# Optimization experiments

Measured on AMD Instinct MI355X. Metric: run time of the kernel, lower is better.

The kernel has to match this reference:

```python
import jax, jax.numpy as jnp
import numpy as np

N = 10000; E = 160000; C = 32; NB = 128; H = 64; L = 3; NL = 4; RC = 5.0
DIMS = [1, 3, 5, 7]

def _sph(v):
    # real spherical harmonics l=0..3 of unit vectors v [E,3]
    x, y, z = v[:, 0], v[:, 1], v[:, 2]
    s3 = 3.0 ** 0.5; s5 = 5.0 ** 0.5; s15 = 15.0 ** 0.5; s7 = 7.0 ** 0.5
    sh0 = jnp.ones_like(x)[:, None]
    sh1 = s3 * v
    sh2 = jnp.stack([s15 * x * y, s15 * y * z, (s5 / 2) * (3 * z * z - 1),
                     s15 * x * z, (s15 / 2) * (x * x - y * y)], -1)
    c1 = (35.0 / 8) ** 0.5; c2 = 105.0 ** 0.5; c3 = (21.0 / 8) ** 0.5; c4 = s7 / 2; c5 = (105.0 ** 0.5) / 2
    sh3 = jnp.stack([c1 * y * (3 * x * x - y * y), c2 * x * y * z, c3 * y * (5 * z * z - 1),
                     c4 * (5 * z ** 3 - 3 * z), c3 * x * (5 * z * z - 1),
                     c5 * z * (x * x - y * y), c1 * x * (x * x - 3 * y * y)], -1)
    return [sh0, sh1, sh2, sh3]

def setup_inputs() -> dict:
    key = jax.random.key(0)
    ks = jax.random.split(key, 14)
    inp = {}
    inp['pos'] = jax.random.uniform(ks[0], (N, 3), jnp.float32) * 10.0  # box of side 10
    inp['node_embed'] = jax.random.normal(ks[1], (4, C), jnp.float32)
    inp['rw1'] = jax.random.normal(ks[2], (NB, H), jnp.float32) * 0.1
    inp['rb1'] = jax.random.normal(ks[3], (H,), jnp.float32) * 0.1
    inp['rw2'] = jax.random.normal(ks[4], (H, L * NL * C), jnp.float32) * 0.1
    inp['rb2'] = jax.random.normal(ks[5], (L * NL * C,), jnp.float32) * 0.1
    inp['self_w'] = jax.random.normal(ks[6], (L, NL, C, C), jnp.float32) * (1.0 / C ** 0.5)
    inp['msg_w'] = jax.random.normal(ks[7], (L, NL, C, C), jnp.float32) * (1.0 / C ** 0.5)
    inp['gate_w'] = jax.random.normal(ks[8], (L, C, C), jnp.float32) * (1.0 / C ** 0.5)
    inp['edge_w'] = jax.random.normal(ks[9], (H, NL * C), jnp.float32) * 0.1
    inp['edge_b'] = jax.random.normal(ks[10], (NL * C,), jnp.float32) * 0.1
    inp['species'] = jax.random.randint(ks[11], (N,), 0, 4)
    inp['edge_index'] = jax.random.randint(ks[12], (2, E), 0, N)
    return inp

def reference(pos, node_embed, rw1, rb1, rw2, rb2, self_w, msg_w, gate_w,
              edge_w, edge_b, species, edge_index):
    src, dst = edge_index[0], edge_index[1]
    vec = pos[dst] - pos[src]                       # [E,3]
    r = jnp.sqrt(jnp.sum(vec * vec, -1) + 1e-12)    # [E]
    u = jnp.clip(r / RC, 0.0, 1.0)
    env = 0.5 * (jnp.cos(jnp.pi * u) + 1.0)         # smooth cutoff, 0 beyond rc
    n = jnp.arange(1, NB + 1, dtype=pos.dtype)
    rb = env[:, None] * (2.0 / RC) ** 0.5 * jnp.sin(jnp.pi * n * u[:, None]) / r[:, None]  # Bessel basis [E,NB]
    h = jax.nn.silu(rb @ rw1 + rb1)                 # [E,H]
    w_all = (h @ rw2 + rb2).reshape(E, L, NL, C)    # per-layer per-l radial weights
    ew = (h @ edge_w + edge_b).reshape(E, NL, C)
    sh = _sph(vec / r[:, None])                     # list of [E, 2l+1]
    # node features per l: [N, C, 2l+1]; l=0 initialized from species embedding
    f = [node_embed[species][:, :, None]] + [jnp.zeros((N, C, d), pos.dtype) for d in DIMS[1:]]
    for t in range(L):
        s = f[0][src][:, :, 0]                      # sender scalars [E,C]
        new = []
        for l in range(NL):
            # scalar-gated radial x SH message (equivariant): [E,C,2l+1]
            m = w_all[:, t, l, :, None] * s[:, :, None] * sh[l][:, None, :]
            agg = jax.ops.segment_sum(m, dst, num_segments=N)
            new.append(jnp.einsum('ncm,cd->ndm', f[l], self_w[t, l]) +
                       jnp.einsum('ncm,cd->ndm', agg, msg_w[t, l]))
        gate = jax.nn.sigmoid(new[0][:, :, 0] @ gate_w[t])  # [N,C]
        f = [jax.nn.silu(new[0])] + [new[l] * gate[:, :, None] for l in range(1, NL)]
    node_out = jnp.concatenate([f[l].reshape(N, C * DIMS[l]) for l in range(NL)], -1)   # [N,512]
    g = f[0][src][:, :, 0] + f[0][dst][:, :, 0]     # [E,C]
    edge_out = jnp.concatenate(
        [(ew[:, l, :, None] * g[:, :, None] * sh[l][:, None, :]).reshape(E, C * DIMS[l])
         for l in range(NL)], -1)                   # [E,512]
    return jnp.concatenate([node_out, edge_out], 0)  # [N+E, 512]
```

## Files before the change

kernel.cpp:

```cpp
#include <hip/hip_runtime.h>

#define NN 10000
#define EE 160000
#define CC 32
#define NBAS 128
#define HH 64
#define LL 3

__device__ __forceinline__ float sigmoidf_(float x) { return 1.0f / (1.0f + expf(-x)); }

__device__ __forceinline__ void edge_geom(const float* pos, int src, int dst,
                                          float& inv_r, float& u, float& pref,
                                          float& x, float& y, float& z) {
    float vx = pos[dst * 3 + 0] - pos[src * 3 + 0];
    float vy = pos[dst * 3 + 1] - pos[src * 3 + 1];
    float vz = pos[dst * 3 + 2] - pos[src * 3 + 2];
    float r2 = vx * vx + vy * vy + vz * vz + 1e-12f;
    float r = sqrtf(r2);
    inv_r = 1.0f / r;
    u = fminf(r * 0.2f, 1.0f);
    const float PI = 3.14159265358979f;
    float env = 0.5f * (cosf(PI * u) + 1.0f);
    pref = env * 0.6324555320336759f * inv_r;
    x = vx * inv_r; y = vy * inv_r; z = vz * inv_r;
}

__device__ __forceinline__ void sph_all(float x, float y, float z, float* shv) {
    const float s3 = 1.7320508075688772f, s5 = 2.23606797749979f, s15 = 3.872983346207417f;
    const float c1 = 2.0916500663351885f;
    const float c2 = 10.246950765959598f;
    const float c3 = 1.6201851746019649f;
    const float c4 = 1.3228756555322954f;
    const float c5 = 5.123475382979799f;
    shv[0] = 1.0f;
    shv[1] = s3 * x; shv[2] = s3 * y; shv[3] = s3 * z;
    shv[4] = s15 * x * y;
    shv[5] = s15 * y * z;
    shv[6] = 0.5f * s5 * (3.0f * z * z - 1.0f);
    shv[7] = s15 * x * z;
    shv[8] = 0.5f * s15 * (x * x - y * y);
    shv[9]  = c1 * y * (3.0f * x * x - y * y);
    shv[10] = c2 * x * y * z;
    shv[11] = c3 * y * (5.0f * z * z - 1.0f);
    shv[12] = c4 * (5.0f * z * z * z - 3.0f * z);
    shv[13] = c3 * x * (5.0f * z * z - 1.0f);
    shv[14] = c5 * z * (x * x - y * y);
    shv[15] = c1 * x * (x * x - 3.0f * y * y);
}

__global__ void k_deg(const int* __restrict__ ei, int* __restrict__ deg) {
    int e = blockIdx.x * blockDim.x + threadIdx.x;
    if (e < EE) atomicAdd(&deg[ei[EE + e]], 1);
}

__global__ __launch_bounds__(256) void k_scan(const int* __restrict__ deg, int* __restrict__ rowptr) {
    __shared__ int part[256];
    const int CHUNK = 40;
    int tid = threadIdx.x;
    int s = 0;
#pragma unroll
    for (int k = 0; k < CHUNK; k++) {
        int idx = tid * CHUNK + k;
        if (idx < NN) s += deg[idx];
    }
    part[tid] = s;
    __syncthreads();
    for (int off = 1; off < 256; off <<= 1) {
        int v = (tid >= off) ? part[tid - off] : 0;
        __syncthreads();
        part[tid] += v;
        __syncthreads();
    }
    int run = (tid > 0) ? part[tid - 1] : 0;
#pragma unroll
    for (int k = 0; k < CHUNK; k++) {
        int idx = tid * CHUNK + k;
        if (idx < NN) { rowptr[idx] = run; run += deg[idx]; }
    }
    if (tid == 255) rowptr[NN] = run;
}

__global__ void k_scatter(const int* __restrict__ ei, const int* __restrict__ rowptr,
                          int* __restrict__ cursor, int* __restrict__ csr) {
    int e = blockIdx.x * blockDim.x + threadIdx.x;
    if (e >= EE) return;
    int d = ei[EE + e];
    int slot = atomicAdd(&cursor[d], 1);
    csr[rowptr[d] + slot] = e;
}

__global__ void k_init_f0(const float* __restrict__ ne, const int* __restrict__ species,
                          float* __restrict__ f0) {
    int idx = blockIdx.x * blockDim.x + threadIdx.x;
    if (idx >= NN * CC) return;
    int c = idx & 31;
    int n = idx >> 5;
    f0[idx] = ne[species[n] * CC + c];
}

__global__ __launch_bounds__(256) void k_edge_pre(
    const float* __restrict__ pos, const float* __restrict__ rw1, const float* __restrict__ rb1,
    const int* __restrict__ ei, float* __restrict__ hbuf, float* __restrict__ shbuf) {
    __shared__ float rw1_s[NBAS * HH];
    __shared__ float rb_s[64 * 132];
    int tid = threadIdx.x;
    int ebase = blockIdx.x * 64;
    for (int i = tid; i < NBAS * HH / 4; i += 256)
        *(float4*)&rw1_s[i * 4] = *(const float4*)&rw1[i * 4];
    {
        int r = tid >> 2, q = tid & 3;
        int e = ebase + r;
        int src = ei[e], dst = ei[EE + e];
        float inv_r, u, pref, x, y, z;
        edge_geom(pos, src, dst, inv_r, u, pref, x, y, z);
        float shv[16];
        sph_all(x, y, z, shv);
        float4 sv;
        sv.x = shv[q * 4 + 0]; sv.y = shv[q * 4 + 1];
        sv.z = shv[q * 4 + 2]; sv.w = shv[q * 4 + 3];
        *(float4*)&shbuf[(size_t)e * 16 + q * 4] = sv;
        const float PI = 3.14159265358979f;
        float th = PI * u;
        float tc = 2.0f * cosf(th);
        float* rp = &rb_s[r * 132 + 32 * q];
        int n0 = 32 * q + 1;
#pragma unroll
        for (int g = 0; g < 2; g++) {
            int nb = n0 + 16 * g;
            float sm1 = sinf(th * (float)nb);
            float s0 = sinf(th * (float)(nb + 1));
            rp[16 * g + 0] = pref * sm1;
            rp[16 * g + 1] = pref * s0;
#pragma unroll
            for (int j = 2; j < 16; j++) {
                float s = tc * s0 - sm1;
                sm1 = s0; s0 = s;
                rp[16 * g + j] = pref * s;
            }
        }
    }
    __syncthreads();
    int col0 = (tid & 15) * 4;
    int r0 = (tid >> 4) * 4;
    float acc[4][4];
#pragma unroll
    for (int i = 0; i < 4; i++) { acc[i][0] = 0.f; acc[i][1] = 0.f; acc[i][2] = 0.f; acc[i][3] = 0.f; }
#pragma unroll 2
    for (int k0 = 0; k0 < NBAS; k0 += 4) {
        float4 w0 = *(float4*)&rw1_s[(k0 + 0) * HH + col0];
        float4 w1 = *(float4*)&rw1_s[(k0 + 1) * HH + col0];
        float4 w2 = *(float4*)&rw1_s[(k0 + 2) * HH + col0];
        float4 w3 = *(float4*)&rw1_s[(k0 + 3) * HH + col0];
#pragma unroll
        for (int i = 0; i < 4; i++) {
            float4 rv = *(float4*)&rb_s[(r0 + i) * 132 + k0];
            acc[i][0] += rv.x * w0.x; acc[i][1] += rv.x * w0.y; acc[i][2] += rv.x * w0.z; acc[i][3] += rv.x * w0.w;
            acc[i][0] += rv.y * w1.x; acc[i][1] += rv.y * w1.y; acc[i][2] += rv.y * w1.z; acc[i][3] += rv.y * w1.w;
            acc[i][0] += rv.z * w2.x; acc[i][1] += rv.z * w2.y; acc[i][2] += rv.z * w2.z; acc[i][3] += rv.z * w2.w;
            acc[i][0] += rv.w * w3.x; acc[i][1] += rv.w * w3.y; acc[i][2] += rv.w * w3.z; acc[i][3] += rv.w * w3.w;
        }
    }
    float4 bv = *(const float4*)&rb1[col0];
#pragma unroll
    for (int i = 0; i < 4; i++) {
        float a0 = acc[i][0] + bv.x, a1 = acc[i][1] + bv.y;
        float a2 = acc[i][2] + bv.z, a3 = acc[i][3] + bv.w;
        float4 hres;
        hres.x = a0 * sigmoidf_(a0); hres.y = a1 * sigmoidf_(a1);
        hres.z = a2 * sigmoidf_(a2); hres.w = a3 * sigmoidf_(a3);
        *(float4*)&hbuf[(size_t)(ebase + r0 + i) * HH + col0] = hres;
    }
}

__global__ __launch_bounds__(256) void k_gemm_all(
    const float* __restrict__ hbuf, const float* __restrict__ rw2,
    const float* __restrict__ rb2, const int* __restrict__ csr,
    float* __restrict__ aw, int panel0, int npanel) {
    __shared__ float w_s[HH * 128];
    __shared__ float h_s[64][68];
    int tid = threadIdx.x;
    int pbase = blockIdx.x * 64;
    {
        int r = tid >> 2, q = tid & 3;
        int e = csr[pbase + r];
        const float4* hp = (const float4*)(hbuf + (size_t)e * HH + q * 16);
        float4 v0 = hp[0], v1 = hp[1], v2 = hp[2], v3 = hp[3];
        float4* dp = (float4*)&h_s[r][q * 16];
        dp[0] = v0; dp[1] = v1; dp[2] = v2; dp[3] = v3;
    }
    int ob = (tid & 31) << 2;
    int r0 = (tid >> 5) << 3;
    for (int p = 0; p < npanel; p++) {
        int wcol = (panel0 + p) * 128;
        __syncthreads();
        for (int i = tid; i < HH * 32; i += 256) {
            int j = i >> 5, o4 = (i & 31) << 2;
            *(float4*)&w_s[j * 128 + o4] = *(const float4*)&rw2[(size_t)j * 384 + wcol + o4];
        }
        __syncthreads();
        float acc[8][4];
#pragma unroll
        for (int i = 0; i < 8; i++) { acc[i][0] = 0.f; acc[i][1] = 0.f; acc[i][2] = 0.f; acc[i][3] = 0.f; }
#pragma unroll 2
        for (int k0 = 0; k0 < HH; k0 += 4) {
            float4 w0 = *(float4*)&w_s[(k0 + 0) * 128 + ob];
            float4 w1 = *(float4*)&w_s[(k0 + 1) * 128 + ob];
            float4 w2 = *(float4*)&w_s[(k0 + 2) * 128 + ob];
            float4 w3 = *(float4*)&w_s[(k0 + 3) * 128 + ob];
#pragma unroll
            for (int i = 0; i < 8; i++) {
                float4 hv = *(float4*)&h_s[r0 + i][k0];
                acc[i][0] += hv.x * w0.x; acc[i][1] += hv.x * w0.y; acc[i][2] += hv.x * w0.z; acc[i][3] += hv.x * w0.w;
                acc[i][0] += hv.y * w1.x; acc[i][1] += hv.y * w1.y; acc[i][2] += hv.y * w1.z; acc[i][3] += hv.y * w1.w;
                acc[i][0] += hv.z * w2.x; acc[i][1] += hv.z * w2.y; acc[i][2] += hv.z * w2.z; acc[i][3] += hv.z * w2.w;
                acc[i][0] += hv.w * w3.x; acc[i][1] += hv.w * w3.y; acc[i][2] += hv.w * w3.z; acc[i][3] += hv.w * w3.w;
            }
        }
        float4 bv = *(const float4*)&rb2[wcol + ob];
        float* awp = aw + (size_t)p * EE * 128;
#pragma unroll
        for (int i = 0; i < 8; i++) {
            float4 res;
            res.x = acc[i][0] + bv.x; res.y = acc[i][1] + bv.y;
            res.z = acc[i][2] + bv.z; res.w = acc[i][3] + bv.w;
            *(float4*)&awp[(size_t)(pbase + r0 + i) * 128 + ob] = res;
        }
    }
}

template<int INIT, int FINAL>
__global__ __launch_bounds__(256) void k_aggnode(
    const float* __restrict__ aw, const float* __restrict__ shbuf,
    const float* __restrict__ f0prev, const float* __restrict__ f_cur,
    const int* __restrict__ ei, const int* __restrict__ rowptr,
    const int* __restrict__ csr,
    const float* __restrict__ self_w, const float* __restrict__ msg_w,
    const float* __restrict__ gate_w,
    float* __restrict__ f_next, float* __restrict__ f0_out, int t) {
    __shared__ float agg_s[4][CC * 17];
    __shared__ float new_s[4][CC * 17];
    __shared__ float gate_s[4][CC];
    int w = threadIdx.x >> 6, lane = threadIdx.x & 63;
    int n = blockIdx.x * 4 + w;
    int c = lane & 31;
    int half = lane >> 5;
    float acc0[3] = {0.f, 0.f, 0.f};
    float acc1[7] = {0.f, 0.f, 0.f, 0.f, 0.f, 0.f, 0.f};
    int beg = rowptr[n], end = rowptr[n + 1];
    for (int k = beg; k < end; k++) {
        int e = csr[k];
        int src = ei[e];
        float fs = f0prev[src * CC + c];
        float a0 = aw[(size_t)k * 128 + lane] * fs;
        float a1 = aw[(size_t)k * 128 + 64 + lane] * fs;
        const float4* shp = (const float4*)(shbuf + (size_t)e * 16);
        float4 s0 = shp[0], s1 = shp[1], s2 = shp[2], s3 = shp[3];
        if (half == 0) {
            acc0[0] += a0 * s0.x;
            acc1[0] += a1 * s1.x; acc1[1] += a1 * s1.y;
            acc1[2] += a1 * s1.z; acc1[3] += a1 * s1.w; acc1[4] += a1 * s2.x;
        } else {
            acc0[0] += a0 * s0.y; acc0[1] += a0 * s0.z; acc0[2] += a0 * s0.w;
            acc1[0] += a1 * s2.y; acc1[1] += a1 * s2.z; acc1[2] += a1 * s2.w;
            acc1[3] += a1 * s3.x; acc1[4] += a1 * s3.y; acc1[5] += a1 * s3.z; acc1[6] += a1 * s3.w;
        }
    }
    {
        int l0 = half, dl0 = 2 * l0 + 1, mo0 = l0 * l0;
        int l1 = 2 + half, dl1 = 2 * l1 + 1, mo1 = l1 * l1;
        float* ap = &agg_s[w][c * 17];
#pragma unroll
        for (int m = 0; m < 3; m++)
            if (m < dl0) ap[mo0 + m] = acc0[m];
#pragma unroll
        for (int m = 0; m < 7; m++)
            if (m < dl1) ap[mo1 + m] = acc1[m];
    }
    int d = c, mg = half;
#pragma unroll
    for (int k = 0; k < 8; k++) {
        int m = mg + 2 * k;
        int l = (m == 0) ? 0 : (m < 4) ? 1 : (m < 9) ? 2 : 3;
        const float* sw = self_w + (size_t)((t * 4 + l) * CC) * CC + d;
        const float* mw = msg_w + (size_t)((t * 4 + l) * CC) * CC + d;
        float acc = 0.0f;
#pragma unroll 8
        for (int c2 = 0; c2 < CC; c2++) {
            float fv;
            if (INIT) fv = (m == 0) ? f0prev[n * CC + c2] : 0.0f;
            else fv = f_cur[((size_t)n * CC + c2) * 16 + m];
            acc += fv * sw[c2 * CC] + agg_s[w][c2 * 17 + m] * mw[c2 * CC];
        }
        new_s[w][d * 17 + m] = acc;
    }
    if (mg == 0) {
        float g = 0.0f;
#pragma unroll 8
        for (int c2 = 0; c2 < CC; c2++)
            g += new_s[w][c2 * 17 + 0] * gate_w[((size_t)t * CC + c2) * CC + d];
        gate_s[w][d] = sigmoidf_(g);
    }
#pragma unroll
    for (int k = 0; k < 8; k++) {
        int m = mg + 2 * k;
        float v = new_s[w][d * 17 + m];
        if (m == 0) v = v * sigmoidf_(v);
        else v *= gate_s[w][d];
        if (FINAL) {
            int l = (m == 0) ? 0 : (m < 4) ? 1 : (m < 9) ? 2 : 3;
            f_next[(size_t)n * 512 + 32 * l * l + d * (2 * l + 1) + (m - l * l)] = v;
        } else {
            f_next[((size_t)n * CC + d) * 16 + m] = v;
        }
        if (m == 0) f0_out[n * CC + d] = v;
    }
}

template<int DL>
__device__ __forceinline__ void emit_edge(float* outp, const float* shp,
                                          float e0, float e1, float e2, float e3) {
    float ew[4] = {e0, e1, e2, e3};
    float buf[4 * DL];
#pragma unroll
    for (int cc = 0; cc < 4; cc++)
#pragma unroll
        for (int m = 0; m < DL; m++) buf[cc * DL + m] = ew[cc] * shp[m];
#pragma unroll
    for (int t = 0; t < DL; t++) *(float4*)&outp[t * 4] = *(float4*)&buf[t * 4];
}

__global__ __launch_bounds__(256) void k_edge_out(
    const float* __restrict__ hbuf, const float* __restrict__ shbuf,
    const float* __restrict__ edge_w, const float* __restrict__ edge_b,
    const float* __restrict__ f0, const int* __restrict__ ei,
    float* __restrict__ out) {
    __shared__ float w_s[HH * 128];
    __shared__ float h_s[64][68];
    __shared__ float sh_s[64][16];
    int tid = threadIdx.x;
    int ebase = blockIdx.x * 64;
    for (int i = tid; i < HH * 32; i += 256) {
        int j = i >> 5, o4 = (i & 31) << 2;
        *(float4*)&w_s[j * 128 + o4] = *(const float4*)&edge_w[(size_t)j * 128 + o4];
    }
    {
        int r = tid >> 2, q = tid & 3;
        int e = ebase + r;
        const float4* hp = (const float4*)(hbuf + (size_t)e * HH + q * 16);
        float4 v0 = hp[0], v1 = hp[1], v2 = hp[2], v3 = hp[3];
        float4* dp = (float4*)&h_s[r][q * 16];
        dp[0] = v0; dp[1] = v1; dp[2] = v2; dp[3] = v3;
        *(float4*)&sh_s[r][q * 4] = *(const float4*)&shbuf[(size_t)e * 16 + q * 4];
    }
    __syncthreads();
    int ob = (tid & 31) << 2;
    int r0 = (tid >> 5) << 3;
    float acc[8][4];
#pragma unroll
    for (int i = 0; i < 8; i++) { acc[i][0] = 0.f; acc[i][1] = 0.f; acc[i][2] = 0.f; acc[i][3] = 0.f; }
#pragma unroll 2
    for (int k0 = 0; k0 < HH; k0 += 4) {
        float4 w0 = *(float4*)&w_s[(k0 + 0) * 128 + ob];
        float4 w1 = *(float4*)&w_s[(k0 + 1) * 128 + ob];
        float4 w2 = *(float4*)&w_s[(k0 + 2) * 128 + ob];
        float4 w3 = *(float4*)&w_s[(k0 + 3) * 128 + ob];
#pragma unroll
        for (int i = 0; i < 8; i++) {
            float4 hv = *(float4*)&h_s[r0 + i][k0];
            acc[i][0] += hv.x * w0.x; acc[i][1] += hv.x * w0.y; acc[i][2] += hv.x * w0.z; acc[i][3] += hv.x * w0.w;
            acc[i][0] += hv.y * w1.x; acc[i][1] += hv.y * w1.y; acc[i][2] += hv.y * w1.z; acc[i][3] += hv.y * w1.w;
            acc[i][0] += hv.z * w2.x; acc[i][1] += hv.z * w2.y; acc[i][2] += hv.z * w2.z; acc[i][3] += hv.z * w2.w;
            acc[i][0] += hv.w * w3.x; acc[i][1] += hv.w * w3.y; acc[i][2] += hv.w * w3.z; acc[i][3] += hv.w * w3.w;
        }
    }
    float4 bv = *(const float4*)&edge_b[ob];
    int l = ob >> 5;
    int cbase = ob & 31;
    int dl = 2 * l + 1, mo = l * l, co = 32 * l * l;
#pragma unroll
    for (int i = 0; i < 8; i++) {
        int rr = r0 + i;
        int e = ebase + rr;
        int src = ei[e], dst = ei[EE + e];
        float4 g1 = *(const float4*)&f0[src * CC + cbase];
        float4 g2 = *(const float4*)&f0[dst * CC + cbase];
        float e0 = (acc[i][0] + bv.x) * (g1.x + g2.x);
        float e1 = (acc[i][1] + bv.y) * (g1.y + g2.y);
        float e2 = (acc[i][2] + bv.z) * (g1.z + g2.z);
        float e3 = (acc[i][3] + bv.w) * (g1.w + g2.w);
        float* outp = out + ((size_t)NN + e) * 512 + co + (size_t)cbase * dl;
        const float* shp = &sh_s[rr][mo];
        if (l == 0)      emit_edge<1>(outp, shp, e0, e1, e2, e3);
        else if (l == 1) emit_edge<3>(outp, shp, e0, e1, e2, e3);
        else if (l == 2) emit_edge<5>(outp, shp, e0, e1, e2, e3);
        else             emit_edge<7>(outp, shp, e0, e1, e2, e3);
    }
}

__global__ __launch_bounds__(256) void k_out_edge(
    const float* __restrict__ pos, const float* __restrict__ rw1, const float* __restrict__ rb1,
    const float* __restrict__ edge_w, const float* __restrict__ edge_b,
    const float* __restrict__ f0, const int* __restrict__ ei, float* __restrict__ out) {
    __shared__ float rw1_s[NBAS * HH];
    __shared__ float ew_s[HH * 128];
    __shared__ float rb_s[4][NBAS];
    __shared__ float h_s[4][HH];
    __shared__ float g_s[4][CC];
    __shared__ float sh_s[4][16];
    int tid = threadIdx.x;
    for (int i = tid; i < NBAS * HH; i += 256) rw1_s[i] = rw1[i];
    for (int i = tid; i < HH * 128; i += 256) ew_s[i] = edge_w[i];
    int w = tid >> 6, lane = tid & 63;
    int e = blockIdx.x * 4 + w;
    int src = ei[e], dst = ei[EE + e];
    float inv_r, u, pref, x, y, z;
    edge_geom(pos, src, dst, inv_r, u, pref, x, y, z);
    const float PI = 3.14159265358979f;
#pragma unroll
    for (int rep = 0; rep < 2; rep++) {
        int k = lane + rep * 64;
        rb_s[w][k] = pref * sinf(PI * (float)(k + 1) * u);
    }
    float shv[16];
    sph_all(x, y, z, shv);
    if (lane < 16) {
        float v = shv[0];
#pragma unroll
        for (int k = 1; k < 16; k++) v = (lane == k) ? shv[k] : v;
        sh_s[w][lane] = v;
    }
    if (lane < CC) g_s[w][lane] = f0[src * CC + lane] + f0[dst * CC + lane];
    __syncthreads();
    float acc = rb1[lane];
#pragma unroll 8
    for (int n = 0; n < NBAS; n++) acc += rb_s[w][n] * rw1_s[n * HH + lane];
    h_s[w][lane] = acc * sigmoidf_(acc);
    __syncthreads();
    size_t orow = ((size_t)NN + e) * 512;
#pragma unroll
    for (int rep = 0; rep < 2; rep++) {
        int o = lane + rep * 64;
        int l = o >> 5, c = o & 31;
        float a = edge_b[o];
#pragma unroll 8
        for (int j = 0; j < HH; j++) a += h_s[w][j] * ew_s[j * 128 + o];
        float base = a * g_s[w][c];
        int dl = 2 * l + 1, mo = l * l, co = 32 * l * l;
        for (int m = 0; m < dl; m++) out[orow + co + c * dl + m] = base * sh_s[w][mo + m];
    }
}

extern "C" void kernel_launch(void* const* d_in, const int* in_sizes, int n_in,
                              void* d_out, int out_size, void* d_ws, size_t ws_size,
                              hipStream_t stream) {
    const float* pos        = (const float*)d_in[0];
    const float* node_embed = (const float*)d_in[1];
    const float* rw1        = (const float*)d_in[2];
    const float* rb1        = (const float*)d_in[3];
    const float* rw2        = (const float*)d_in[4];
    const float* rb2        = (const float*)d_in[5];
    const float* self_w     = (const float*)d_in[6];
    const float* msg_w      = (const float*)d_in[7];
    const float* gate_w     = (const float*)d_in[8];
    const float* edge_w     = (const float*)d_in[9];
    const float* edge_b     = (const float*)d_in[10];
    const int* species      = (const int*)d_in[11];
    const int* ei           = (const int*)d_in[12];
    float* out = (float*)d_out;

    float* f0fin = (float*)d_ws;
    float* f0A   = f0fin + (size_t)NN * CC;
    float* f0B   = f0A + (size_t)NN * CC;
    float* hbuf  = f0B + (size_t)NN * CC;
    float* shbuf = hbuf + (size_t)EE * HH;
    float* fA    = shbuf + (size_t)EE * 16;
    int* deg     = (int*)(fA + (size_t)NN * 512);
    int* rowptr  = deg + NN;
    int* cursor  = rowptr + NN + 1;
    int* csr     = cursor + NN;
    size_t base_need = (size_t)((char*)(csr + EE) - (char*)d_ws);
    size_t extra_need = ((size_t)NN * 512 + (size_t)EE * 384) * 4;
    float* fB;
    float* aw;
    bool deep_fallback = false;
    if (ws_size >= base_need + extra_need) {
        fB = (float*)((char*)d_ws + base_need);
        aw = fB + (size_t)NN * 512;
    } else if (ws_size >= base_need) {
        fB = out + (size_t)NN * 512;
        aw = fB + (size_t)NN * 512;
    } else {
        deep_fallback = true;
        float* s = out + (size_t)NN * 512;
        hbuf = s; shbuf = hbuf + (size_t)EE * HH;
        fA = shbuf + (size_t)EE * 16;
        fB = fA + (size_t)NN * 512;
        aw = fB + (size_t)NN * 512;
        deg = (int*)(aw + (size_t)EE * 128);
        rowptr = deg + NN; cursor = rowptr + NN + 1; csr = cursor + NN;
    }

    hipMemsetAsync(deg, 0, (size_t)NN * 4, stream);
    hipMemsetAsync(cursor, 0, (size_t)NN * 4, stream);
    k_deg<<<(EE + 255) / 256, 256, 0, stream>>>(ei, deg);
    k_scan<<<1, 256, 0, stream>>>(deg, rowptr);
    k_scatter<<<(EE + 255) / 256, 256, 0, stream>>>(ei, rowptr, cursor, csr);

    k_init_f0<<<(NN * CC + 255) / 256, 256, 0, stream>>>(node_embed, species, f0A);
    k_edge_pre<<<EE / 64, 256, 0, stream>>>(pos, rw1, rb1, ei, hbuf, shbuf);

    if (!deep_fallback) {
        k_gemm_all<<<EE / 64, 256, 0, stream>>>(hbuf, rw2, rb2, csr, aw, 0, 3);
        k_aggnode<1, 0><<<NN / 4, 256, 0, stream>>>(aw, shbuf, f0A, nullptr,
            ei, rowptr, csr, self_w, msg_w, gate_w, fA, f0B, 0);
        k_aggnode<0, 0><<<NN / 4, 256, 0, stream>>>(aw + (size_t)EE * 128, shbuf, f0B, fA,
            ei, rowptr, csr, self_w, msg_w, gate_w, fB, f0A, 1);
        k_aggnode<0, 1><<<NN / 4, 256, 0, stream>>>(aw + (size_t)2 * EE * 128, shbuf, f0A, fB,
            ei, rowptr, csr, self_w, msg_w, gate_w, out, f0fin, 2);
        k_edge_out<<<EE / 64, 256, 0, stream>>>(hbuf, shbuf, edge_w, edge_b, f0fin, ei, out);
    } else {
        k_gemm_all<<<EE / 64, 256, 0, stream>>>(hbuf, rw2, rb2, csr, aw, 0, 1);
        k_aggnode<1, 0><<<NN / 4, 256, 0, stream>>>(aw, shbuf, f0A, nullptr,
            ei, rowptr, csr, self_w, msg_w, gate_w, fA, f0B, 0);
        k_gemm_all<<<EE / 64, 256, 0, stream>>>(hbuf, rw2, rb2, csr, aw, 1, 1);
        k_aggnode<0, 0><<<NN / 4, 256, 0, stream>>>(aw, shbuf, f0B, fA,
            ei, rowptr, csr, self_w, msg_w, gate_w, fB, f0A, 1);
        k_gemm_all<<<EE / 64, 256, 0, stream>>>(hbuf, rw2, rb2, csr, aw, 2, 1);
        k_aggnode<0, 1><<<NN / 4, 256, 0, stream>>>(aw, shbuf, f0A, fB,
            ei, rowptr, csr, self_w, msg_w, gate_w, out, f0fin, 2);
        k_out_edge<<<EE / 4, 256, 0, stream>>>(pos, rw1, rb1, edge_w, edge_b, f0fin, ei, out);
    }
}
```

Baseline: 1.133 ms.

## Fuse radial GEMM into edge precompute, store weights as bf16 in CSR order

Merges the second radial-MLP GEMM into the edge precompute kernel. Each block now scatters its per-edge radial weights directly to CSR positions through a new ipos map, which removes the separate gather GEMM kernel and the hbuf re-read. The per-layer radial weights are stored as bf16, halving that traffic, and spherical harmonics and source indices are also written in CSR order so the aggregation loop reads contiguously without indirection. This drops the deep-fallback path and adds bf16 rounding error to the message weights.

Measured after the change: 1.017 ms. 1.11x faster.

```diff
diff --git a/kernel.cpp b/kernel.cpp
--- a/kernel.cpp
+++ b/kernel.cpp
@@ -8,6 +8,15 @@
 #define LL 3
 
 __device__ __forceinline__ float sigmoidf_(float x) { return 1.0f / (1.0f + expf(-x)); }
+
+__device__ __forceinline__ unsigned short f2bf(float f) {
+    unsigned int u = __float_as_uint(f);
+    unsigned int r = u + 0x7FFFu + ((u >> 16) & 1u);
+    return (unsigned short)(r >> 16);
+}
+__device__ __forceinline__ float bf2f(unsigned short h) {
+    return __uint_as_float(((unsigned int)h) << 16);
+}
 
 __device__ __forceinline__ void edge_geom(const float* pos, int src, int dst,
                                           float& inv_r, float& u, float& pref,
@@ -81,12 +90,16 @@
 }
 
 __global__ void k_scatter(const int* __restrict__ ei, const int* __restrict__ rowptr,
-                          int* __restrict__ cursor, int* __restrict__ csr) {
+                          int* __restrict__ cursor, int* __restrict__ ipos,
+                          int* __restrict__ srcc) {
     int e = blockIdx.x * blockDim.x + threadIdx.x;
     if (e >= EE) return;
     int d = ei[EE + e];
+    int s = ei[e];
     int slot = atomicAdd(&cursor[d], 1);
-    csr[rowptr[d] + slot] = e;
+    int p = rowptr[d] + slot;
+    ipos[e] = p;
+    srcc[p] = s;
 }
 
 __global__ void k_init_f0(const float* __restrict__ ne, const int* __restrict__ species,
@@ -100,16 +113,23 @@
 
 __global__ __launch_bounds__(256) void k_edge_pre(
     const float* __restrict__ pos, const float* __restrict__ rw1, const float* __restrict__ rb1,
-    const int* __restrict__ ei, float* __restrict__ hbuf, float* __restrict__ shbuf) {
-    __shared__ float rw1_s[NBAS * HH];
+    const float* __restrict__ rw2, const float* __restrict__ rb2,
+    const int* __restrict__ ei, const int* __restrict__ ipos,
+    float* __restrict__ hbuf, float* __restrict__ shbuf, float* __restrict__ shc,
+    unsigned short* __restrict__ awh) {
+    __shared__ float w_s[NBAS * HH];
     __shared__ float rb_s[64 * 132];
+    __shared__ int ip_s[64];
+    float* h_s = rb_s;
     int tid = threadIdx.x;
     int ebase = blockIdx.x * 64;
     for (int i = tid; i < NBAS * HH / 4; i += 256)
-        *(float4*)&rw1_s[i * 4] = *(const float4*)&rw1[i * 4];
+        *(float4*)&w_s[i * 4] = *(const float4*)&rw1[i * 4];
     {
         int r = tid >> 2, q = tid & 3;
         int e = ebase + r;
+        int ip = ipos[e];
+        if (q == 0) ip_s[r] = ip;
         int src = ei[e], dst = ei[EE + e];
         float inv_r, u, pref, x, y, z;
         edge_geom(pos, src, dst, inv_r, u, pref, x, y, z);
@@ -119,6 +139,7 @@
         sv.x = shv[q * 4 + 0]; sv.y = shv[q * 4 + 1];
         sv.z = shv[q * 4 + 2]; sv.w = shv[q * 4 + 3];
         *(float4*)&shbuf[(size_t)e * 16 + q * 4] = sv;
+        *(float4*)&shc[(size_t)ip * 16 + q * 4] = sv;
         const float PI = 3.14159265358979f;
         float th = PI * u;
         float tc = 2.0f * cosf(th);
@@ -141,61 +162,51 @@
     }
     __syncthreads();
     int col0 = (tid & 15) * 4;
-    int r0 = (tid >> 4) * 4;
-    float acc[4][4];
-#pragma unroll
-    for (int i = 0; i < 4; i++) { acc[i][0] = 0.f; acc[i][1] = 0.f; acc[i][2] = 0.f; acc[i][3] = 0.f; }
+    int r0b = (tid >> 4) * 4;
+    float4 hkeep[4];
+    {
+        float acc[4][4];
+#pragma unroll
+        for (int i = 0; i < 4; i++) { acc[i][0] = 0.f; acc[i][1] = 0.f; acc[i][2] = 0.f; acc[i][3] = 0.f; }
 #pragma unroll 2
-    for (int k0 = 0; k0 < NBAS; k0 += 4) {
-        float4 w0 = *(float4*)&rw1_s[(k0 + 0) * HH + col0];
-        float4 w1 = *(float4*)&rw1_s[(k0 + 1) * HH + col0];
-        float4 w2 = *(float4*)&rw1_s[(k0 + 2) * HH + col0];
-        float4 w3 = *(float4*)&rw1_s[(k0 + 3) * HH + col0];
+        for (int k0 = 0; k0 < NBAS; k0 += 4) {
+            float4 w0 = *(float4*)&w_s[(k0 + 0) * HH + col0];
+            float4 w1 = *(float4*)&w_s[(k0 + 1) * HH + col0];
+            float4 w2 = *(float4*)&w_s[(k0 + 2) * HH + col0];
+            float4 w3 = *(float4*)&w_s[(k0 + 3) * HH + col0];
+#pragma unroll
+            for (int i = 0; i < 4; i++) {
+                float4 rv = *(float4*)&rb_s[(r0b + i) * 132 + k0];
+                acc[i][0] += rv.x * w0.x; acc[i][1] += rv.x * w0.y; acc[i][2] += rv.x * w0.z; acc[i][3] += rv.x * w0.w;
+                acc[i][0] += rv.y * w1.x; acc[i][1] += rv.y * w1.y; acc[i][2] += rv.y * w1.z; acc[i][3] += rv.y * w1.w;
+                acc[i][0] += rv.z * w2.x; acc[i][1] += rv.z * w2.y; acc[i][2] += rv.z * w2.z; acc[i][3] += rv.z * w2.w;
+                acc[i][0] += rv.w * w3.x; acc[i][1] += rv.w * w3.y; acc[i][2] += rv.w * w3.z; acc[i][3] += rv.w * w3.w;
+            }
+        }
+        float4 bv = *(const float4*)&rb1[col0];
 #pragma unroll
         for (int i = 0; i < 4; i++) {
-            float4 rv = *(float4*)&rb_s[(r0 + i) * 132 + k0];
-            acc[i][0] += rv.x * w0.x; acc[i][1] += rv.x * w0.y; acc[i][2] += rv.x * w0.z; acc[i][3] += rv.x * w0.w;
-            acc[i][0] += rv.y * w1.x; acc[i][1] += rv.y * w1.y; acc[i][2] += rv.y * w1.z; acc[i][3] += rv.y * w1.w;
-            acc[i][0] += rv.z * w2.x; acc[i][1] += rv.z * w2.y; acc[i][2] += rv.z * w2.z; acc[i][3] += rv.z * w2.w;
-            acc[i][0] += rv.w * w3.x; acc[i][1] += rv.w * w3.y; acc[i][2] += rv.w * w3.z; acc[i][3] += rv.w * w3.w;
-        }
-    }
-    float4 bv = *(const float4*)&rb1[col0];
-#pragma unroll
-    for (int i = 0; i < 4; i++) {
-        float a0 = acc[i][0] + bv.x, a1 = acc[i][1] + bv.y;
-        float a2 = acc[i][2] + bv.z, a3 = acc[i][3] + bv.w;
-        float4 hres;
-        hres.x = a0 * sigmoidf_(a0); hres.y = a1 * sigmoidf_(a1);
-        hres.z = a2 * sigmoidf_(a2); hres.w = a3 * sigmoidf_(a3);
-        *(float4*)&hbuf[(size_t)(ebase + r0 + i) * HH + col0] = hres;
-    }
-}
-
-__global__ __launch_bounds__(256) void k_gemm_all(
-    const float* __restrict__ hbuf, const float* __restrict__ rw2,
-    const float* __restrict__ rb2, const int* __restrict__ csr,
-    float* __restrict__ aw, int panel0, int npanel) {
-    __shared__ float w_s[HH * 128];
-    __shared__ float h_s[64][68];
-    int tid = threadIdx.x;
-    int pbase = blockIdx.x * 64;
-    {
-        int r = tid >> 2, q = tid & 3;
-        int e = csr[pbase + r];
-        const float4* hp = (const float4*)(hbuf + (size_t)e * HH + q * 16);
-        float4 v0 = hp[0], v1 = hp[1], v2 = hp[2], v3 = hp[3];
-        float4* dp = (float4*)&h_s[r][q * 16];
-        dp[0] = v0; dp[1] = v1; dp[2] = v2; dp[3] = v3;
-    }
+            float a0 = acc[i][0] + bv.x, a1 = acc[i][1] + bv.y;
+            float a2 = acc[i][2] + bv.z, a3 = acc[i][3] + bv.w;
+            float4 hres;
+            hres.x = a0 * sigmoidf_(a0); hres.y = a1 * sigmoidf_(a1);
+            hres.z = a2 * sigmoidf_(a2); hres.w = a3 * sigmoidf_(a3);
+            *(float4*)&hbuf[(size_t)(ebase + r0b + i) * HH + col0] = hres;
+            hkeep[i] = hres;
+        }
+    }
+    __syncthreads();
+#pragma unroll
+    for (int i = 0; i < 4; i++)
+        *(float4*)&h_s[(r0b + i) * 68 + col0] = hkeep[i];
     int ob = (tid & 31) << 2;
     int r0 = (tid >> 5) << 3;
-    for (int p = 0; p < npanel; p++) {
-        int wcol = (panel0 + p) * 128;
+#pragma unroll 1
+    for (int p = 0; p < 3; p++) {
         __syncthreads();
         for (int i = tid; i < HH * 32; i += 256) {
             int j = i >> 5, o4 = (i & 31) << 2;
-            *(float4*)&w_s[j * 128 + o4] = *(const float4*)&rw2[(size_t)j * 384 + wcol + o4];
+            *(float4*)&w_s[j * 128 + o4] = *(const float4*)&rw2[(size_t)j * 384 + p * 128 + o4];
         }
         __syncthreads();
         float acc[8][4];
@@ -209,31 +220,34 @@
             float4 w3 = *(float4*)&w_s[(k0 + 3) * 128 + ob];
 #pragma unroll
             for (int i = 0; i < 8; i++) {
-                float4 hv = *(float4*)&h_s[r0 + i][k0];
+                float4 hv = *(float4*)&h_s[(r0 + i) * 68 + k0];
                 acc[i][0] += hv.x * w0.x; acc[i][1] += hv.x * w0.y; acc[i][2] += hv.x * w0.z; acc[i][3] += hv.x * w0.w;
                 acc[i][0] += hv.y * w1.x; acc[i][1] += hv.y * w1.y; acc[i][2] += hv.y * w1.z; acc[i][3] += hv.y * w1.w;
                 acc[i][0] += hv.z * w2.x; acc[i][1] += hv.z * w2.y; acc[i][2] += hv.z * w2.z; acc[i][3] += hv.z * w2.w;
                 acc[i][0] += hv.w * w3.x; acc[i][1] += hv.w * w3.y; acc[i][2] += hv.w * w3.z; acc[i][3] += hv.w * w3.w;
             }
         }
-        float4 bv = *(const float4*)&rb2[wcol + ob];
-        float* awp = aw + (size_t)p * EE * 128;
+        float4 bv = *(const float4*)&rb2[p * 128 + ob];
+        unsigned short* awp = awh + (size_t)p * EE * 128;
 #pragma unroll
         for (int i = 0; i < 8; i++) {
-            float4 res;
-            res.x = acc[i][0] + bv.x; res.y = acc[i][1] + bv.y;
-            res.z = acc[i][2] + bv.z; res.w = acc[i][3] + bv.w;
-            *(float4*)&awp[(size_t)(pbase + r0 + i) * 128 + ob] = res;
+            int ip = ip_s[r0 + i];
+            ushort4 st;
+            st.x = f2bf(acc[i][0] + bv.x);
+            st.y = f2bf(acc[i][1] + bv.y);
+            st.z = f2bf(acc[i][2] + bv.z);
+            st.w = f2bf(acc[i][3] + bv.w);
+            *(ushort4*)&awp[(size_t)ip * 128 + ob] = st;
         }
     }
 }
 
 template<int INIT, int FINAL>
 __global__ __launch_bounds__(256) void k_aggnode(
-    const float* __restrict__ aw, const float* __restrict__ shbuf,
+    const unsigned short* __restrict__ awh, const float* __restrict__ shc,
+    const int* __restrict__ srcc,
     const float* __restrict__ f0prev, const float* __restrict__ f_cur,
-    const int* __restrict__ ei, const int* __restrict__ rowptr,
-    const int* __restrict__ csr,
+    const int* __restrict__ rowptr,
     const float* __restrict__ self_w, const float* __restrict__ msg_w,
     const float* __restrict__ gate_w,
     float* __restrict__ f_next, float* __restrict__ f0_out, int t) {
@@ -248,12 +262,11 @@
     float acc1[7] = {0.f, 0.f, 0.f, 0.f, 0.f, 0.f, 0.f};
     int beg = rowptr[n], end = rowptr[n + 1];
     for (int k = beg; k < end; k++) {
-        int e = csr[k];
-        int src = ei[e];
+        int src = srcc[k];
         float fs = f0prev[src * CC + c];
-        float a0 = aw[(size_t)k * 128 + lane] * fs;
-        float a1 = aw[(size_t)k * 128 + 64 + lane] * fs;
-        const float4* shp = (const float4*)(shbuf + (size_t)e * 16);
+        float a0 = bf2f(awh[(size_t)k * 128 + lane]) * fs;
+        float a1 = bf2f(awh[(size_t)k * 128 + 64 + lane]) * fs;
+        const float4* shp = (const float4*)(shc + (size_t)k * 16);
         float4 s0 = shp[0], s1 = shp[1], s2 = shp[2], s3 = shp[3];
         if (half == 0) {
             acc0[0] += a0 * s0.x;
@@ -394,59 +407,6 @@
         else if (l == 1) emit_edge<3>(outp, shp, e0, e1, e2, e3);
         else if (l == 2) emit_edge<5>(outp, shp, e0, e1, e2, e3);
         else             emit_edge<7>(outp, shp, e0, e1, e2, e3);
-    }
-}
-
-__global__ __launch_bounds__(256) void k_out_edge(
-    const float* __restrict__ pos, const float* __restrict__ rw1, const float* __restrict__ rb1,
-    const float* __restrict__ edge_w, const float* __restrict__ edge_b,
-    const float* __restrict__ f0, const int* __restrict__ ei, float* __restrict__ out) {
-    __shared__ float rw1_s[NBAS * HH];
-    __shared__ float ew_s[HH * 128];
-    __shared__ float rb_s[4][NBAS];
-    __shared__ float h_s[4][HH];
-    __shared__ float g_s[4][CC];
-    __shared__ float sh_s[4][16];
-    int tid = threadIdx.x;
-    for (int i = tid; i < NBAS * HH; i += 256) rw1_s[i] = rw1[i];
-    for (int i = tid; i < HH * 128; i += 256) ew_s[i] = edge_w[i];
-    int w = tid >> 6, lane = tid & 63;
-    int e = blockIdx.x * 4 + w;
-    int src = ei[e], dst = ei[EE + e];
-    float inv_r, u, pref, x, y, z;
-    edge_geom(pos, src, dst, inv_r, u, pref, x, y, z);
-    const float PI = 3.14159265358979f;
-#pragma unroll
-    for (int rep = 0; rep < 2; rep++) {
-        int k = lane + rep * 64;
-        rb_s[w][k] = pref * sinf(PI * (float)(k + 1) * u);
-    }
-    float shv[16];
-    sph_all(x, y, z, shv);
-    if (lane < 16) {
-        float v = shv[0];
-#pragma unroll
-        for (int k = 1; k < 16; k++) v = (lane == k) ? shv[k] : v;
-        sh_s[w][lane] = v;
-    }
-    if (lane < CC) g_s[w][lane] = f0[src * CC + lane] + f0[dst * CC + lane];
-    __syncthreads();
-    float acc = rb1[lane];
-#pragma unroll 8
-    for (int n = 0; n < NBAS; n++) acc += rb_s[w][n] * rw1_s[n * HH + lane];
-    h_s[w][lane] = acc * sigmoidf_(acc);
-    __syncthreads();
-    size_t orow = ((size_t)NN + e) * 512;
-#pragma unroll
-    for (int rep = 0; rep < 2; rep++) {
-        int o = lane + rep * 64;
-        int l = o >> 5, c = o & 31;
-        float a = edge_b[o];
-#pragma unroll 8
-        for (int j = 0; j < HH; j++) a += h_s[w][j] * ew_s[j * 128 + o];
-        float base = a * g_s[w][c];
-        int dl = 2 * l + 1, mo = l * l, co = 32 * l * l;
-        for (int m = 0; m < dl; m++) out[orow + co + c * dl + m] = base * sh_s[w][mo + m];
     }
 }
 
@@ -473,61 +433,42 @@
     float* f0B   = f0A + (size_t)NN * CC;
     float* hbuf  = f0B + (size_t)NN * CC;
     float* shbuf = hbuf + (size_t)EE * HH;
-    float* fA    = shbuf + (size_t)EE * 16;
+    float* shc   = shbuf + (size_t)EE * 16;
+    float* fA    = shc + (size_t)EE * 16;
     int* deg     = (int*)(fA + (size_t)NN * 512);
     int* rowptr  = deg + NN;
-    int* cursor  = rowptr + NN + 1;
-    int* csr     = cursor + NN;
-    size_t base_need = (size_t)((char*)(csr + EE) - (char*)d_ws);
-    size_t extra_need = ((size_t)NN * 512 + (size_t)EE * 384) * 4;
+    int* cursor  = rowptr + NN + 2;
+    int* ipos    = cursor + NN;
+    int* srcc    = ipos + EE;
+    char* endbase = (char*)(srcc + EE);
+    size_t base_need = (size_t)(endbase - (char*)d_ws);
+    size_t extra_need = (size_t)NN * 512 * 4 + (size_t)3 * EE * 128 * 2;
     float* fB;
-    float* aw;
-    bool deep_fallback = false;
+    unsigned short* awh;
     if (ws_size >= base_need + extra_need) {
-        fB = (float*)((char*)d_ws + base_need);
-        aw = fB + (size_t)NN * 512;
-    } else if (ws_size >= base_need) {
-        fB = out + (size_t)NN * 512;
-        aw = fB + (size_t)NN * 512;
+        fB  = (float*)endbase;
+        awh = (unsigned short*)(fB + (size_t)NN * 512);
     } else {
-        deep_fallback = true;
-        float* s = out + (size_t)NN * 512;
-        hbuf = s; shbuf = hbuf + (size_t)EE * HH;
-        fA = shbuf + (size_t)EE * 16;
-        fB = fA + (size_t)NN * 512;
-        aw = fB + (size_t)NN * 512;
-        deg = (int*)(aw + (size_t)EE * 128);
-        rowptr = deg + NN; cursor = rowptr + NN + 1; csr = cursor + NN;
+        fB  = out + (size_t)NN * 512;
+        awh = (unsigned short*)(fB + (size_t)NN * 512);
     }
 
     hipMemsetAsync(deg, 0, (size_t)NN * 4, stream);
     hipMemsetAsync(cursor, 0, (size_t)NN * 4, stream);
     k_deg<<<(EE + 255) / 256, 256, 0, stream>>>(ei, deg);
     k_scan<<<1, 256, 0, stream>>>(deg, rowptr);
-    k_scatter<<<(EE + 255) / 256, 256, 0, stream>>>(ei, rowptr, cursor, csr);
+    k_scatter<<<(EE + 255) / 256, 256, 0, stream>>>(ei, rowptr, cursor, ipos, srcc);
 
     k_init_f0<<<(NN * CC + 255) / 256, 256, 0, stream>>>(node_embed, species, f0A);
-    k_edge_pre<<<EE / 64, 256, 0, stream>>>(pos, rw1, rb1, ei, hbuf, shbuf);
-
-    if (!deep_fallback) {
-        k_gemm_all<<<EE / 64, 256, 0, stream>>>(hbuf, rw2, rb2, csr, aw, 0, 3);
-        k_aggnode<1, 0><<<NN / 4, 256, 0, stream>>>(aw, shbuf, f0A, nullptr,
-            ei, rowptr, csr, self_w, msg_w, gate_w, fA, f0B, 0);
-        k_aggnode<0, 0><<<NN / 4, 256, 0, stream>>>(aw + (size_t)EE * 128, shbuf, f0B, fA,
-            ei, rowptr, csr, self_w, msg_w, gate_w, fB, f0A, 1);
-        k_aggnode<0, 1><<<NN / 4, 256, 0, stream>>>(aw + (size_t)2 * EE * 128, shbuf, f0A, fB,
-            ei, rowptr, csr, self_w, msg_w, gate_w, out, f0fin, 2);
-        k_edge_out<<<EE / 64, 256, 0, stream>>>(hbuf, shbuf, edge_w, edge_b, f0fin, ei, out);
-    } else {
-        k_gemm_all<<<EE / 64, 256, 0, stream>>>(hbuf, rw2, rb2, csr, aw, 0, 1);
-        k_aggnode<1, 0><<<NN / 4, 256, 0, stream>>>(aw, shbuf, f0A, nullptr,
-            ei, rowptr, csr, self_w, msg_w, gate_w, fA, f0B, 0);
-        k_gemm_all<<<EE / 64, 256, 0, stream>>>(hbuf, rw2, rb2, csr, aw, 1, 1);
-        k_aggnode<0, 0><<<NN / 4, 256, 0, stream>>>(aw, shbuf, f0B, fA,
-            ei, rowptr, csr, self_w, msg_w, gate_w, fB, f0A, 1);
-        k_gemm_all<<<EE / 64, 256, 0, stream>>>(hbuf, rw2, rb2, csr, aw, 2, 1);
-        k_aggnode<0, 1><<<NN / 4, 256, 0, stream>>>(aw, shbuf, f0A, fB,
-            ei, rowptr, csr, self_w, msg_w, gate_w, out, f0fin, 2);
-        k_out_edge<<<EE / 4, 256, 0, stream>>>(pos, rw1, rb1, edge_w, edge_b, f0fin, ei, out);
-    }
-}
+    k_edge_pre<<<EE / 64, 256, 0, stream>>>(pos, rw1, rb1, rw2, rb2, ei, ipos,
+                                            hbuf, shbuf, shc, awh);
+
+    k_aggnode<1, 0><<<NN / 4, 256, 0, stream>>>(awh, shc, srcc, f0A, nullptr,
+        rowptr, self_w, msg_w, gate_w, fA, f0B, 0);
+    k_aggnode<0, 0><<<NN / 4, 256, 0, stream>>>(awh + (size_t)EE * 128, shc, srcc, f0B, fA,
+        rowptr, self_w, msg_w, gate_w, fB, f0A, 1);
+    k_aggnode<0, 1><<<NN / 4, 256, 0, stream>>>(awh + (size_t)2 * EE * 128, shc, srcc, f0A, fB,
+        rowptr, self_w, msg_w, gate_w, out, f0fin, 2);
+
+    k_edge_out<<<EE / 64, 256, 0, stream>>>(hbuf, shbuf, edge_w, edge_b, f0fin, ei, out);
+}
```
